# Kernel optimization log

Measured on AMD Instinct MI355X. Metric: run time of the kernel, lower is better.

## Reference

```python
import jax, jax.numpy as jnp
import numpy as np

C = 16      # internal_channel
G = 8       # deform groups
KK = 9      # 3x3 kernel taps


def conv2d(x, w, b, pad):
    y = jax.lax.conv_general_dilated(
        x, w, window_strides=(1, 1), padding=[(pad, pad), (pad, pad)],
        dimension_numbers=('NCHW', 'OIHW', 'NCHW'))
    return y + b[None, :, None, None]


def feature_extraction(img, p):
    f1 = jax.nn.relu(conv2d(img, p['conv1_w'], p['conv1_b'], 1))   # [B,C,H,W]
    f2 = jax.nn.relu(conv2d(f1, p['conv2_w'], p['conv2_b'], 0))    # [B,C,H-2,W-2]
    f3 = jax.nn.relu(conv2d(f2, p['conv3_w'], p['conv3_b'], 0))    # [B,C,H-4,W-4]
    return [f1, f2, f3]


def deform_conv2d(x, offset, w, b, groups):
    # torchvision deform_conv2d semantics: stride 1, pad 1, dilation 1, 3x3,
    # zero out-of-bounds bilinear sampling, explicit offsets.
    B, Ci, H, W = x.shape
    Cg = Ci // groups
    off = offset.reshape(B, groups, KK, 2, H, W)
    oy, ox = off[:, :, :, 0], off[:, :, :, 1]          # [B,G,K,H,W]
    k = jnp.arange(KK)
    ky = (k // 3).reshape(1, 1, KK, 1, 1).astype(x.dtype)
    kx = (k % 3).reshape(1, 1, KK, 1, 1).astype(x.dtype)
    hh = jnp.arange(H, dtype=x.dtype).reshape(1, 1, 1, H, 1)
    ww = jnp.arange(W, dtype=x.dtype).reshape(1, 1, 1, 1, W)
    ys = hh - 1.0 + ky + oy                            # sample rows
    xs = ww - 1.0 + kx + ox                            # sample cols
    y0 = jnp.floor(ys); x0 = jnp.floor(xs)
    dy = ys - y0; dx = xs - x0
    y0i = y0.astype(jnp.int32); x0i = x0.astype(jnp.int32)
    xg = x.reshape(B, groups, Cg, H * W)

    def gather(iy, ix):
        valid = ((iy >= 0) & (iy < H) & (ix >= 0) & (ix < W)).astype(x.dtype)
        idx = jnp.clip(iy, 0, H - 1) * W + jnp.clip(ix, 0, W - 1)
        g = jnp.take_along_axis(xg, idx.reshape(B, groups, 1, KK * H * W), axis=3)
        return g.reshape(B, groups, Cg, KK, H, W) * valid[:, :, None]

    v = (gather(y0i, x0i) * ((1 - dy) * (1 - dx))[:, :, None]
         + gather(y0i, x0i + 1) * ((1 - dy) * dx)[:, :, None]
         + gather(y0i + 1, x0i) * (dy * (1 - dx))[:, :, None]
         + gather(y0i + 1, x0i + 1) * (dy * dx)[:, :, None])
    v = v.reshape(B, Ci, KK, H, W)
    out = jnp.einsum('ocK,bcKhw->bohw', w.reshape(w.shape[0], Ci, KK), v)
    return out + b[None, :, None, None]


def setup_inputs() -> dict:
    key = jax.random.key(0)
    ks = jax.random.split(key, 12)
    B, H, Wd = 4, 256, 256
    d = {
        'ref_image': jax.random.normal(ks[0], (B, 3, H, Wd), jnp.float32),
        'unreg_image': jax.random.normal(ks[1], (B, 3, H, Wd), jnp.float32),
        'conv1_w': jax.random.normal(ks[2], (C, 3, 3, 3), jnp.float32) * 0.05,
        'conv1_b': jnp.zeros((C,), jnp.float32),
        'conv2_w': jax.random.normal(ks[3], (C, C, 3, 3), jnp.float32) * 0.05,
        'conv2_b': jnp.zeros((C,), jnp.float32),
        'conv3_w': jax.random.normal(ks[4], (C, C, 3, 3), jnp.float32) * 0.05,
        'conv3_b': jnp.zeros((C,), jnp.float32),
        'off1_w': jax.random.normal(ks[5], (2 * G * KK, 2 * C, 3, 3), jnp.float32) * 0.01,
        'off1_b': jnp.zeros((2 * G * KK,), jnp.float32),
        'off2_w': jax.random.normal(ks[6], (2 * G * KK, 2 * C, 3, 3), jnp.float32) * 0.01,
        'off2_b': jnp.zeros((2 * G * KK,), jnp.float32),
        'off3_w': jax.random.normal(ks[7], (2 * G * KK, 2 * C, 3, 3), jnp.float32) * 0.01,
        'off3_b': jnp.zeros((2 * G * KK,), jnp.float32),
        'dcn_w': jax.random.normal(ks[8], (C, C, 3, 3), jnp.float32) * 0.05,
        'dcn_b': jnp.zeros((C,), jnp.float32),
    }
    return d


def reference(ref_image, unreg_image, conv1_w, conv1_b, conv2_w, conv2_b,
              conv3_w, conv3_b, off1_w, off1_b, off2_w, off2_b,
              off3_w, off3_b, dcn_w, dcn_b):
    p = dict(conv1_w=conv1_w, conv1_b=conv1_b, conv2_w=conv2_w, conv2_b=conv2_b,
             conv3_w=conv3_w, conv3_b=conv3_b)
    ref_f = feature_extraction(ref_image, p)
    unr_f = feature_extraction(unreg_image, p)
    off_ws = [(off1_w, off1_b), (off2_w, off2_b), (off3_w, off3_b)]
    aligned = []
    for i in range(3):
        cat = jnp.concatenate([ref_f[i], unr_f[i]], axis=1)          # [B,2C,Hi,Wi]
        offset = jax.nn.relu(conv2d(cat, off_ws[i][0], off_ws[i][1], 1))
        aligned.append(deform_conv2d(unr_f[i], offset, dcn_w, dcn_b, G))
    return tuple(aligned)
```

## Files before the change

### kernel.cpp

```cpp
#include <hip/hip_runtime.h>


typedef __attribute__((ext_vector_type(8))) short bf16x8;
typedef __attribute__((ext_vector_type(4))) float f32x4;
typedef __attribute__((ext_vector_type(2))) float f32x2;

__device__ inline unsigned short f2bf(float f) {
    union { float f; unsigned int u; } x; x.f = f;
    unsigned int u = x.u;
    u += 0x7fffu + ((u >> 16) & 1u);
    return (unsigned short)(u >> 16);
}
__device__ inline float bf2f(unsigned short u) {
    union { unsigned int i; float f; } x; x.i = ((unsigned int)u) << 16;
    return x.f;
}
__device__ inline f32x2 ld2(const float* p) {
    f32x2 v;
    __builtin_memcpy(&v, p, 8);
    return v;
}

__device__ inline void xcd_swz(int& bx, int& by, int& bz) {
    const int gx = gridDim.x, gy = gridDim.y, gz = gridDim.z;
    const int hw = blockIdx.x + gx * (blockIdx.y + gy * blockIdx.z);
    const int per = (gx * gy * gz) >> 3;
    const int lg = (hw & 7) * per + (hw >> 3);
    bz = lg / (gx * gy);
    const int rem = lg - bz * gx * gy;
    by = rem / gx;
    bx = rem - by * gx;
}

__global__ __launch_bounds__(256) void conv1_kernel(
    const float* __restrict__ ref, const float* __restrict__ unr,
    const float* __restrict__ w, const float* __restrict__ bias,
    unsigned short* __restrict__ outA, unsigned short* __restrict__ outB,
    float* __restrict__ pU)
{
    const int H = 256, W = 256;
    __shared__ float sIn[3][18][18];
    const int tx = threadIdx.x, ty = threadIdx.y;
    const int tid = ty * 16 + tx;
    const int bx = blockIdx.x, by = blockIdx.y, bz8 = blockIdx.z;
    const int isUnr = bz8 >> 2, bb = bz8 & 3;
    const float* in = isUnr ? unr : ref;
    unsigned short* outCL = isUnr ? outB : outA;
    const int x0 = bx * 16 - 1, y0 = by * 16 - 1;

    for (int idx = tid; idx < 3 * 324; idx += 256) {
        int c = idx / 324, rem = idx % 324, r = rem / 18, col = rem % 18;
        int gy = y0 + r, gx = x0 + col;
        float v = 0.f;
        if (gy >= 0 && gy < H && gx >= 0 && gx < W)
            v = in[((bb * 3 + c) * H + gy) * W + gx];
        sIn[c][r][col] = v;
    }
    __syncthreads();

    const int y = by * 16 + ty, x = bx * 16 + tx;
    float acc[16];
#pragma unroll
    for (int o = 0; o < 16; o++) acc[o] = bias[o];
#pragma unroll
    for (int ci = 0; ci < 3; ci++) {
        float xv[9];
#pragma unroll
        for (int r = 0; r < 3; r++)
#pragma unroll
            for (int c = 0; c < 3; c++)
                xv[r * 3 + c] = sIn[ci][ty + r][tx + c];
#pragma unroll
        for (int o = 0; o < 16; o++) {
            const float* wp = w + (o * 3 + ci) * 9;
#pragma unroll
            for (int u = 0; u < 9; u++) acc[o] += wp[u] * xv[u];
        }
    }
#pragma unroll
    for (int o = 0; o < 16; o++) acc[o] = fmaxf(acc[o], 0.f);

    const size_t HW = (size_t)H * W;
    unsigned short tmp[16];
#pragma unroll
    for (int o = 0; o < 16; o++) tmp[o] = f2bf(acc[o]);
    unsigned short* op = outCL + ((size_t)bb * HW + (size_t)y * W + x) * 16;
    *(bf16x8*)(op) = *(bf16x8*)&tmp[0];
    *(bf16x8*)(op + 8) = *(bf16x8*)&tmp[8];
    if (isUnr) {
#pragma unroll
        for (int o = 0; o < 16; o++)
            pU[((size_t)(bb * 16 + o) * H + y) * W + x] = acc[o];
    }
}

__global__ __launch_bounds__(512, 4) void c16m_kernel(
    const unsigned short* __restrict__ inA, const unsigned short* __restrict__ inB,
    const unsigned short* __restrict__ Bc16, const float* __restrict__ bias,
    unsigned short* __restrict__ outA, unsigned short* __restrict__ outB,
    float* __restrict__ pU, int Hout, int Wout)
{
    const int Hin = Hout + 2, Win = Wout + 2;
    __shared__ __align__(16) unsigned short sC[324 * 16];
    __shared__ float sT[16][16][17];
    const int tid = threadIdx.x;
    const int bx = blockIdx.x, by = blockIdx.y, bz8 = blockIdx.z;
    const int isUnr = bz8 >> 2, bz = bz8 & 3;
    const unsigned short* inCL = isUnr ? inB : inA;
    unsigned short* outCL = isUnr ? outB : outA;
    const int x0 = bx * 16, y0 = by * 16;

    for (int idx = tid; idx < 648; idx += 512) {
        int px = idx >> 1, half = idx & 1;
        int r = px / 18, c = px % 18;
        int gy = min(y0 + r, Hin - 1), gx = min(x0 + c, Win - 1);
        const bf16x8* p = (const bf16x8*)(inCL +
            (((size_t)bz * Hin * Win + (size_t)gy * Win + gx) * 16 + 8 * half));
        *(bf16x8*)&sC[px * 16 + 8 * half] = *p;
    }
    __syncthreads();

    const int w = tid >> 6, l = tid & 63;
    const int q = l >> 4, j16 = l & 15;
    const float bv = bias[j16];
    f32x4 acc0 = {bv, bv, bv, bv}, acc1 = {bv, bv, bv, bv};

#pragma unroll
    for (int t = 0; t < 5; ++t) {
        const int u = (t == 4) ? 8 : 2 * t + (q >> 1);
        const int dr = u / 3, dc = u % 3;
        bf16x8 a0 = *(const bf16x8*)&sC[(((w) + dr) * 18 + (j16 + dc)) * 16 + (q & 1) * 8];
        bf16x8 a1 = *(const bf16x8*)&sC[(((w + 8) + dr) * 18 + (j16 + dc)) * 16 + (q & 1) * 8];
        bf16x8 b = *(const bf16x8*)&Bc16[(t * 64 + l) * 8];
        acc0 = __builtin_amdgcn_mfma_f32_16x16x32_bf16(a0, b, acc0, 0, 0, 0);
        acc1 = __builtin_amdgcn_mfma_f32_16x16x32_bf16(a1, b, acc1, 0, 0, 0);
    }
#pragma unroll
    for (int r = 0; r < 4; ++r) { acc0[r] = fmaxf(acc0[r], 0.f); acc1[r] = fmaxf(acc1[r], 0.f); }

    const int yA = y0 + w, yB = y0 + w + 8;
    const size_t HWo = (size_t)Hout * Wout;
#pragma unroll
    for (int r = 0; r < 4; ++r) {
        int x = x0 + 4 * q + r;
        if (yA < Hout && x < Wout)
            outCL[((size_t)bz * HWo + (size_t)yA * Wout + x) * 16 + j16] = f2bf(acc0[r]);
        if (yB < Hout && x < Wout)
            outCL[((size_t)bz * HWo + (size_t)yB * Wout + x) * 16 + j16] = f2bf(acc1[r]);
    }

    if (isUnr) {
#pragma unroll
        for (int r = 0; r < 4; ++r) {
            sT[w][j16][4 * q + r] = acc0[r];
            sT[w + 8][j16][4 * q + r] = acc1[r];
        }
        __syncthreads();
        const int ch = tid >> 5, yy = (tid >> 1) & 15, half = tid & 1;
        const int yo = y0 + yy;
        if (yo < Hout) {
            float* dst = pU + ((size_t)(bz * 16 + ch) * Hout + yo) * Wout + x0 + half * 8;
#pragma unroll
            for (int i = 0; i < 8; ++i) {
                int x = x0 + half * 8 + i;
                if (x < Wout) dst[i] = sT[yy][ch][half * 8 + i];
            }
        }
    }
}

__global__ __launch_bounds__(512) void prep_kernel(
    const float* __restrict__ o1w, const float* __restrict__ o2w, const float* __restrict__ o3w,
    const float* __restrict__ o1b, const float* __restrict__ o2b, const float* __restrict__ o3b,
    const float* __restrict__ dw, const float* __restrict__ c2w, const float* __restrict__ c3w,
    unsigned short* __restrict__ Bfrag, float* __restrict__ biasPrep,
    unsigned short* __restrict__ Bc16, unsigned short* __restrict__ dwB)
{
    const int lvl = blockIdx.y;
    const float* Wt = (lvl == 0) ? o1w : (lvl == 1) ? o2w : o3w;
    const float* Bb = (lvl == 0) ? o1b : (lvl == 1) ? o2b : o3b;
    int idx = blockIdx.x * 512 + threadIdx.x;
    int j = idx & 7;
    int l = (idx >> 3) & 63;
    int tu = idx >> 9;
    int t = tu / 9, u = tu % 9;
    int q = l >> 4, n16 = l & 15;
    int ci = 8 * q + j;
    int g = n16 >> 1, d = n16 & 1;
    int ch = g * 18 + t * 2 + d;
    Bfrag[lvl * 41472 + idx] = f2bf(Wt[(ch * 32 + ci) * 9 + u]);
    if (blockIdx.x == 0 && threadIdx.x < 144) {
        int n = threadIdx.x;
        int tt = n >> 4, nn = n & 15;
        biasPrep[lvl * 144 + n] = Bb[(nn >> 1) * 18 + tt * 2 + (nn & 1)];
    }
    if (lvl == 0 && blockIdx.x == 1) {
        for (int i = threadIdx.x; i < 2560; i += 512) {
            int jj = i & 7, l2 = (i >> 3) & 63, chn = i >> 9;
            int q2 = l2 >> 4, o = l2 & 15;
            int kkl = 8 * q2 + jj;
            int gg = kkl >> 2, tl = (kkl >> 1) & 1, dd = kkl & 1;
            int tt = 2 * chn + tl, cc = 2 * gg + dd;
            float val = (tt < 9) ? dw[(o * 16 + cc) * 9 + tt] : 0.f;
            dwB[i] = f2bf(val);
        }
    }
    if (lvl == 2 && blockIdx.x >= 20 && blockIdx.x < 30) {
        int i2 = (blockIdx.x - 20) * 512 + threadIdx.x;
        int cw = i2 / 2560, rem = i2 % 2560;
        int jj = rem & 7, ll = (rem >> 3) & 63, tt = rem >> 9;
        int qq = ll >> 4, oo = ll & 15;
        int uu = (tt == 4) ? 8 : 2 * tt + (qq >> 1);
        int cc = (qq & 1) * 8 + jj;
        const float* wsel = cw ? c3w : c2w;
        float val = (tt == 4 && qq >= 2) ? 0.f : wsel[(oo * 16 + cc) * 9 + uu];
        Bc16[i2] = f2bf(val);
    }
}

#define CP 40
__global__ __launch_bounds__(512, 4) void offconv_kernel(
    const unsigned short* __restrict__ refCL, const unsigned short* __restrict__ unrCL,
    const unsigned short* __restrict__ Bfrag, const float* __restrict__ biasPrep,
    unsigned short* __restrict__ offbuf, int bbBase, int BN, int H, int W)
{
    __shared__ __align__(16) unsigned short sIn[18 * 18 * CP];
    __shared__ __align__(16) unsigned short sB[2][4608];
    const int tid = threadIdx.x;
    int bx, by, bz;
    xcd_swz(bx, by, bz);
    const int bb = bbBase + bz;
    const int x0 = bx * 16 - 1, y0 = by * 16 - 1;
    const size_t HW = (size_t)H * W;

    auto loadB = [&](int t, int buf) {
        const bf16x8* src = (const bf16x8*)(Bfrag + (size_t)t * 4608);
        bf16x8* dst = (bf16x8*)&sB[buf][0];
        dst[tid] = src[tid];
        if (tid < 64) dst[512 + tid] = src[512 + tid];
    };
    loadB(0, 0);

    for (int idx = tid; idx < 1296; idx += 512) {
        int px = idx >> 2, ch8 = idx & 3;
        int r = px / 18, c = px % 18;
        int gy = y0 + r, gx = x0 + c;
        bf16x8 v = {};
        if (gy >= 0 && gy < H && gx >= 0 && gx < W) {
            const unsigned short* src = (ch8 < 2) ? refCL : unrCL;
            v = *(const bf16x8*)(src + (((size_t)bb * HW + (size_t)gy * W + gx) * 16 + (ch8 & 1) * 8));
        }
        *(bf16x8*)&sIn[px * CP + ch8 * 8] = v;
    }
    __syncthreads();

    const int w = tid >> 6, l = tid & 63;
    const int q = l >> 4, j16 = l & 15;

    bf16x8 a0[9], a1[9];
#pragma unroll
    for (int u = 0; u < 9; ++u) {
        int dr = u / 3, dc = u % 3;
        a0[u] = *(const bf16x8*)&sIn[((w + dr) * 18 + (j16 + dc)) * CP + 8 * q];
        a1[u] = *(const bf16x8*)&sIn[((w + 8 + dr) * 18 + (j16 + dc)) * CP + 8 * q];
    }
    const int yA = by * 16 + w, yB = by * 16 + w + 8;

    float bvv[9];
#pragma unroll
    for (int t = 0; t < 9; ++t) bvv[t] = biasPrep[t * 16 + j16];

#pragma unroll 1
    for (int t = 0; t < 9; ++t) {
        if (t < 8) loadB(t + 1, (t + 1) & 1);
        const unsigned short* bp = &sB[t & 1][0];
        const float bv = bvv[t];
        f32x4 acc0 = {bv, bv, bv, bv}, acc1 = {bv, bv, bv, bv};
#pragma unroll
        for (int u = 0; u < 9; ++u) {
            bf16x8 b = *(const bf16x8*)&bp[(u * 64 + l) * 8];
            acc0 = __builtin_amdgcn_mfma_f32_16x16x32_bf16(a0[u], b, acc0, 0, 0, 0);
            acc1 = __builtin_amdgcn_mfma_f32_16x16x32_bf16(a1[u], b, acc1, 0, 0, 0);
        }
        const size_t tb = ((size_t)t * BN + bz) * HW;
#pragma unroll
        for (int r = 0; r < 4; ++r) {
            int x = bx * 16 + 4 * q + r;
            if (yA < H && x < W)
                offbuf[(tb + (size_t)yA * W + x) * 16 + j16] = f2bf(fmaxf(acc0[r], 0.f));
            if (yB < H && x < W)
                offbuf[(tb + (size_t)yB * W + x) * 16 + j16] = f2bf(fmaxf(acc1[r], 0.f));
        }
        __syncthreads();
    }
}

__global__ __launch_bounds__(256) void deform_kernel(
    const float* __restrict__ unrP, const unsigned short* __restrict__ offbuf,
    const unsigned short* __restrict__ dwB, const float* __restrict__ dcn_b,
    float* __restrict__ out, int bbBase, int BN, int H, int W)
{
    __shared__ __align__(16) unsigned int sA[256 * 20];
    const int tid = threadIdx.x;
    const int tx = tid & 15, ty = tid >> 4;
    int bxs, bys, bz;
    xcd_swz(bxs, bys, bz);
    const int bb = bbBase + bz;
    const int xr = bxs * 16 + tx, yr = bys * 16 + ty;
    const int x = min(xr, W - 1), y = min(yr, H - 1);
    const size_t HW = (size_t)H * W;
    const float* base = unrP + (size_t)bb * 16 * HW;
    const size_t pxi = (size_t)y * W + x;

    const int wv = tid >> 6, l = tid & 63, q = l >> 4, j16 = l & 15;
    const float bvb = dcn_b[j16];
    f32x4 acc0 = {bvb, bvb, bvb, bvb}, acc1 = acc0, acc2 = acc0, acc3 = acc0;

#pragma unroll 1
    for (int chn = 0; chn < 5; ++chn) {
#pragma unroll
        for (int tl = 0; tl < 2; ++tl) {
            const int t = 2 * chn + tl;
            if (t < 9) {
                const unsigned short* po = offbuf + (((size_t)t * BN + bz) * HW + pxi) * 16;
                bf16x8 s0 = *(const bf16x8*)(po);
                bf16x8 s1 = *(const bf16x8*)(po + 8);
                float ov[16];
#pragma unroll
                for (int i = 0; i < 8; ++i) ov[i] = bf2f((unsigned short)s0[i]);
#pragma unroll
                for (int i = 0; i < 8; ++i) ov[8 + i] = bf2f((unsigned short)s1[i]);

                const float fy = (float)(y - 1 + t / 3);
                const float fx = (float)(x - 1 + t % 3);
#pragma unroll
                for (int g = 0; g < 8; ++g) {
                    float oy = ov[2 * g], ox = ov[2 * g + 1];
                    float ys = fy + oy, xs = fx + ox;
                    float y0f = floorf(ys), x0f = floorf(xs);
                    float dy = ys - y0f, dx = xs - x0f;
                    int iy0 = (int)y0f, ix0 = (int)x0f;
                    int iy1 = iy0 + 1, ix1 = ix0 + 1;
                    float vy0 = (iy0 >= 0 && iy0 < H) ? 1.f : 0.f;
                    float vy1 = (iy1 >= 0 && iy1 < H) ? 1.f : 0.f;
                    float vx0 = (ix0 >= 0 && ix0 < W) ? 1.f : 0.f;
                    float vx1 = (ix1 < W) ? 1.f : 0.f;
                    int pb = min(max(ix0, 0), W - 2);
                    const bool swp = (ix0 != pb);
                    float wx0 = (1.f - dx) * vx0, wx1 = dx * vx1;
                    float wA = swp ? wx1 : wx0;
                    float wB = swp ? wx0 : wx1;
                    float wy0 = (1.f - dy) * vy0, wy1 = dy * vy1;
                    int cy0 = min(max(iy0, 0), H - 1), cy1 = min(max(iy1, 0), H - 1);
                    const float* p0 = base + (size_t)(2 * g) * HW;
                    const float* p1 = base + (size_t)(2 * g + 1) * HW;
                    const int ib0 = cy0 * W + pb, ib1 = cy1 * W + pb;
                    f32x2 a0 = ld2(p0 + ib0), a1 = ld2(p0 + ib1);
                    f32x2 b0 = ld2(p1 + ib0), b1 = ld2(p1 + ib1);
                    float wA0 = wy0 * wA, wB0 = wy0 * wB, wA1 = wy1 * wA, wB1 = wy1 * wB;
                    float v0 = wA0 * a0.x + wB0 * a0.y + wA1 * a1.x + wB1 * a1.y;
                    float v1 = wA0 * b0.x + wB0 * b0.y + wA1 * b1.x + wB1 * b1.y;
                    sA[tid * 20 + g * 2 + tl] =
                        (unsigned int)f2bf(v0) | ((unsigned int)f2bf(v1) << 16);
                }
            } else {
#pragma unroll
                for (int g = 0; g < 8; ++g) sA[tid * 20 + g * 2 + tl] = 0u;
            }
        }
        __syncthreads();
        bf16x8 b = *(const bf16x8*)((const unsigned short*)dwB + (size_t)(chn * 64 + l) * 8);
        {
            bf16x8 a;
            a = *(const bf16x8*)&sA[((4 * wv + 0) * 16 + j16) * 20 + 4 * q];
            acc0 = __builtin_amdgcn_mfma_f32_16x16x32_bf16(a, b, acc0, 0, 0, 0);
            a = *(const bf16x8*)&sA[((4 * wv + 1) * 16 + j16) * 20 + 4 * q];
            acc1 = __builtin_amdgcn_mfma_f32_16x16x32_bf16(a, b, acc1, 0, 0, 0);
            a = *(const bf16x8*)&sA[((4 * wv + 2) * 16 + j16) * 20 + 4 * q];
            acc2 = __builtin_amdgcn_mfma_f32_16x16x32_bf16(a, b, acc2, 0, 0, 0);
            a = *(const bf16x8*)&sA[((4 * wv + 3) * 16 + j16) * 20 + 4 * q];
            acc3 = __builtin_amdgcn_mfma_f32_16x16x32_bf16(a, b, acc3, 0, 0, 0);
        }
        __syncthreads();
    }

    unsigned int* sT = sA;
#pragma unroll
    for (int r = 0; r < 4; ++r) {
        union { float f; unsigned int u; } cvt;
        cvt.f = acc0[r]; sT[((4 * wv + 0) * 16 + 4 * q + r) * 17 + j16] = cvt.u;
        cvt.f = acc1[r]; sT[((4 * wv + 1) * 16 + 4 * q + r) * 17 + j16] = cvt.u;
        cvt.f = acc2[r]; sT[((4 * wv + 2) * 16 + 4 * q + r) * 17 + j16] = cvt.u;
        cvt.f = acc3[r]; sT[((4 * wv + 3) * 16 + 4 * q + r) * 17 + j16] = cvt.u;
    }
    __syncthreads();

    if (xr < W && yr < H) {
#pragma unroll
        for (int o = 0; o < 16; ++o) {
            union { unsigned int u; float f; } cvt;
            cvt.u = sT[tid * 17 + o];
            out[((size_t)(bb * 16 + o) * H + y) * W + x] = cvt.f;
        }
    }
}

extern "C" void kernel_launch(void* const* d_in, const int* in_sizes, int n_in,
                              void* d_out, int out_size, void* d_ws, size_t ws_size,
                              hipStream_t stream) {
    (void)in_sizes; (void)n_in; (void)out_size;
    const float* ref = (const float*)d_in[0];
    const float* unr = (const float*)d_in[1];
    const float* c1w = (const float*)d_in[2];  const float* c1b = (const float*)d_in[3];
    const float* c2w = (const float*)d_in[4];  const float* c2b = (const float*)d_in[5];
    const float* c3w = (const float*)d_in[6];  const float* c3b = (const float*)d_in[7];
    const float* o1w = (const float*)d_in[8];  const float* o1b = (const float*)d_in[9];
    const float* o2w = (const float*)d_in[10]; const float* o2b = (const float*)d_in[11];
    const float* o3w = (const float*)d_in[12]; const float* o3b = (const float*)d_in[13];
    const float* dw  = (const float*)d_in[14]; const float* db  = (const float*)d_in[15];

    float* out0 = (float*)d_out;
    float* out1 = out0 + (size_t)4 * 16 * 256 * 256;
    float* out2 = out1 + (size_t)4 * 16 * 254 * 254;

    unsigned short* fA = (unsigned short*)d_ws;
    unsigned short* fB = fA + (size_t)4 * 65536 * 16;
    unsigned short* fC = fB + (size_t)4 * 65536 * 16;
    unsigned short* fD = fC + (size_t)4 * 64516 * 16;
    float* pU = (float*)(fD + (size_t)4 * 64516 * 16);
    unsigned short* BfragBase = (unsigned short*)(pU + (size_t)4 * 16 * 65536);
    unsigned short* Bc16 = BfragBase + 3 * 41472;
    unsigned short* dwB = Bc16 + 2 * 2560;
    float* biasPrep = (float*)(dwB + 2560);
    unsigned short* offbuf = (unsigned short*)(biasPrep + 3 * 144);

    const size_t used = (size_t)((char*)offbuf - (char*)d_ws);
    const size_t slice1 = (size_t)256 * 256 * 144;
    const int NB = (ws_size >= used + 4 * slice1 * 2) ? 4 : 1;

    dim3 blk(16, 16);
    prep_kernel<<<dim3(81, 3), 512, 0, stream>>>(o1w, o2w, o3w, o1b, o2b, o3b,
                                                 dw, c2w, c3w,
                                                 BfragBase, biasPrep, Bc16, dwB);
    conv1_kernel<<<dim3(16, 16, 8), blk, 0, stream>>>(ref, unr, c1w, c1b, fA, fB, pU);

    for (int lvl = 0; lvl < 3; ++lvl) {
        const unsigned short *rf, *uf; float* o; int H;
        const unsigned short* Bf = BfragBase + lvl * 41472;
        const float* bp = biasPrep + lvl * 144;
        if (lvl == 0) { rf = fA; uf = fB; o = out0; H = 256; }
        else if (lvl == 1) { rf = fC; uf = fD; o = out1; H = 254; }
        else { rf = fA; uf = fB; o = out2; H = 252; }

        if (NB == 4) {
            offconv_kernel<<<dim3(16, 16, 4), 512, 0, stream>>>(rf, uf, Bf, bp, offbuf, 0, 4, H, H);
            deform_kernel<<<dim3(16, 16, 4), 256, 0, stream>>>(pU, offbuf, dwB, db, o, 0, 4, H, H);
        } else {
            for (int b = 0; b < 4; ++b) {
                offconv_kernel<<<dim3(16, 16, 1), 512, 0, stream>>>(rf, uf, Bf, bp, offbuf, b, 1, H, H);
                deform_kernel<<<dim3(16, 16, 1), 256, 0, stream>>>(pU, offbuf, dwB, db, o, b, 1, H, H);
            }
        }

        if (lvl == 0) {
            c16m_kernel<<<dim3(16, 16, 8), 512, 0, stream>>>(fA, fB, Bc16, c2b, fC, fD, pU, 254, 254);
        } else if (lvl == 1) {
            c16m_kernel<<<dim3(16, 16, 8), 512, 0, stream>>>(fC, fD, Bc16 + 2560, c3b, fA, fB, pU, 252, 252);
        }
    }
}
```

Measured before the change: 307.6 us.

## Double-buffer deform sampling LDS tile and swizzle its layout

Double-buffers the LDS staging tile in the deform kernel so the bilinear sampling for the next channel chunk is written while the current chunk feeds the MFMAs. This drops one barrier per iteration. It also applies an XOR swizzle to the LDS addresses to reduce bank conflicts on the 16-byte A-fragment reads. LDS use doubles, which may lower occupancy, and the swizzle has to stay consistent between writes and reads.

```diff
diff --git a/kernel.cpp b/kernel.cpp
--- a/kernel.cpp
+++ b/kernel.cpp
@@ -300,7 +300,7 @@
     const unsigned short* __restrict__ dwB, const float* __restrict__ dcn_b,
     float* __restrict__ out, int bbBase, int BN, int H, int W)
 {
-    __shared__ __align__(16) unsigned int sA[256 * 20];
+    __shared__ __align__(16) unsigned int sA[2][256 * 20];
     const int tid = threadIdx.x;
     const int tx = tid & 15, ty = tid >> 4;
     int bxs, bys, bz;
@@ -316,8 +316,9 @@
     const float bvb = dcn_b[j16];
     f32x4 acc0 = {bvb, bvb, bvb, bvb}, acc1 = acc0, acc2 = acc0, acc3 = acc0;
 
-#pragma unroll 1
-    for (int chn = 0; chn < 5; ++chn) {
+    auto swz = [](int R, int c) { return (R * 20 + c) ^ (((R >> 3) & 3) << 2); };
+
+    auto stage = [&](int chn, int buf) {
 #pragma unroll
         for (int tl = 0; tl < 2; ++tl) {
             const int t = 2 * chn + tl;
@@ -355,36 +356,42 @@
                     const float* p0 = base + (size_t)(2 * g) * HW;
                     const float* p1 = base + (size_t)(2 * g + 1) * HW;
                     const int ib0 = cy0 * W + pb, ib1 = cy1 * W + pb;
-                    f32x2 a0 = ld2(p0 + ib0), a1 = ld2(p0 + ib1);
-                    f32x2 b0 = ld2(p1 + ib0), b1 = ld2(p1 + ib1);
+                    f32x2 a0v = ld2(p0 + ib0), a1v = ld2(p0 + ib1);
+                    f32x2 b0v = ld2(p1 + ib0), b1v = ld2(p1 + ib1);
                     float wA0 = wy0 * wA, wB0 = wy0 * wB, wA1 = wy1 * wA, wB1 = wy1 * wB;
-                    float v0 = wA0 * a0.x + wB0 * a0.y + wA1 * a1.x + wB1 * a1.y;
-                    float v1 = wA0 * b0.x + wB0 * b0.y + wA1 * b1.x + wB1 * b1.y;
-                    sA[tid * 20 + g * 2 + tl] =
+                    float v0 = wA0 * a0v.x + wB0 * a0v.y + wA1 * a1v.x + wB1 * a1v.y;
+                    float v1 = wA0 * b0v.x + wB0 * b0v.y + wA1 * b1v.x + wB1 * b1v.y;
+                    sA[buf][swz(tid, g * 2 + tl)] =
                         (unsigned int)f2bf(v0) | ((unsigned int)f2bf(v1) << 16);
                 }
             } else {
 #pragma unroll
-                for (int g = 0; g < 8; ++g) sA[tid * 20 + g * 2 + tl] = 0u;
+                for (int g = 0; g < 8; ++g) sA[buf][swz(tid, g * 2 + tl)] = 0u;
             }
         }
+    };
+
+    stage(0, 0);
+    __syncthreads();
+
+#pragma unroll 1
+    for (int chn = 0; chn < 5; ++chn) {
+        if (chn < 4) stage(chn + 1, (chn + 1) & 1);
+        const unsigned int* cb = &sA[chn & 1][0];
+        bf16x8 b = *(const bf16x8*)((const unsigned short*)dwB + (size_t)(chn * 64 + l) * 8);
+        bf16x8 a;
+        a = *(const bf16x8*)&cb[swz((4 * wv + 0) * 16 + j16, 4 * q)];
+        acc0 = __builtin_amdgcn_mfma_f32_16x16x32_bf16(a, b, acc0, 0, 0, 0);
+        a = *(const bf16x8*)&cb[swz((4 * wv + 1) * 16 + j16, 4 * q)];
+        acc1 = __builtin_amdgcn_mfma_f32_16x16x32_bf16(a, b, acc1, 0, 0, 0);
+        a = *(const bf16x8*)&cb[swz((4 * wv + 2) * 16 + j16, 4 * q)];
+        acc2 = __builtin_amdgcn_mfma_f32_16x16x32_bf16(a, b, acc2, 0, 0, 0);
+        a = *(const bf16x8*)&cb[swz((4 * wv + 3) * 16 + j16, 4 * q)];
+        acc3 = __builtin_amdgcn_mfma_f32_16x16x32_bf16(a, b, acc3, 0, 0, 0);
         __syncthreads();
-        bf16x8 b = *(const bf16x8*)((const unsigned short*)dwB + (size_t)(chn * 64 + l) * 8);
-        {
-            bf16x8 a;
-            a = *(const bf16x8*)&sA[((4 * wv + 0) * 16 + j16) * 20 + 4 * q];
-            acc0 = __builtin_amdgcn_mfma_f32_16x16x32_bf16(a, b, acc0, 0, 0, 0);
-            a = *(const bf16x8*)&sA[((4 * wv + 1) * 16 + j16) * 20 + 4 * q];
-            acc1 = __builtin_amdgcn_mfma_f32_16x16x32_bf16(a, b, acc1, 0, 0, 0);
-            a = *(const bf16x8*)&sA[((4 * wv + 2) * 16 + j16) * 20 + 4 * q];
-            acc2 = __builtin_amdgcn_mfma_f32_16x16x32_bf16(a, b, acc2, 0, 0, 0);
-            a = *(const bf16x8*)&sA[((4 * wv + 3) * 16 + j16) * 20 + 4 * q];
-            acc3 = __builtin_amdgcn_mfma_f32_16x16x32_bf16(a, b, acc3, 0, 0, 0);
-        }
-        __syncthreads();
-    }
-
-    unsigned int* sT = sA;
+    }
+
+    unsigned int* sT = &sA[0][0];
 #pragma unroll
     for (int r = 0; r < 4; ++r) {
         union { float f; unsigned int u; } cvt;
```

New measurement: 308.7 us. No clear change (+0.3%).
